# Optimization experiments

Hardware: AMD Instinct MI355X
Metric: run time of the kernel (lower is better)

The kernel has to match this reference:

```python
import jax, jax.numpy as jnp
import numpy as np

# Static config matching init_kwargs / forward constants
H = 12          # num_heads
D = 64          # head_dim
SW = 64         # kv_cache_sliding_window (frames)
SF = 8          # kv_cache_scale_frames
NUM_REG = 4     # num_register_tokens -> camera_idx=0, scale_idx=5
SPECIAL_END = NUM_REG + 2  # camera..scale inclusive slice = tokens [0:6)


def setup_inputs() -> dict:
    key = jax.random.key(0)
    ks = jax.random.split(key, 9)
    B, N, C = 1, 576, 768
    T = 192  # tokens per frame; num_frame_per_block = N // T = 3
    inp = {
        'x': jax.random.normal(ks[0], (B, N, C), jnp.float32),
        'qkv_w': jax.random.normal(ks[1], (3 * C, C), jnp.float32) * (C ** -0.5),
        'qkv_b': jax.random.normal(ks[2], (3 * C,), jnp.float32) * 0.02,
        'proj_w': jax.random.normal(ks[3], (C, C), jnp.float32) * (C ** -0.5),
        'proj_b': jax.random.normal(ks[4], (C,), jnp.float32) * 0.02,
        'k_cache': jax.random.normal(ks[5], (B, H, SW + SF, T, D), jnp.float32),
        'v_cache': jax.random.normal(ks[6], (B, H, SW + SF, T, D), jnp.float32),
        'k_special': jax.random.normal(ks[7], (B, H, 12, SPECIAL_END, D), jnp.float32),
        'v_special': jax.random.normal(ks[8], (B, H, 12, SPECIAL_END, D), jnp.float32),
    }
    return inp


def reference(x, qkv_w, qkv_b, proj_w, proj_b, k_cache, v_cache, k_special, v_special):
    B, N, C = x.shape
    T = k_cache.shape[3]           # tokens per frame
    nfb = N // T                   # num_frame_per_block (inferred, as in torch code)

    # qkv projection: (B,N,3C) -> (3,B,H,N,D)
    qkv = (x @ qkv_w.T + qkv_b).reshape(B, N, 3, H, D).transpose(2, 0, 3, 1, 4)
    q, k, v = qkv[0], qkv[1], qkv[2]   # each (B,H,N,D); q_norm/k_norm = Identity

    # Append new block frames to the cache
    k_cache = jnp.concatenate([k_cache, k.reshape(B, H, nfb, T, D)], axis=2)
    v_cache = jnp.concatenate([v_cache, v.reshape(B, H, nfb, T, D)], axis=2)

    # Sliding-window eviction (shapes chosen so this branch always fires)
    F = k_cache.shape[2]
    evict_start, evict_end = SF, F - SW   # 8 .. 11
    # cross-frame special tokens: camera..scale (tokens 0:6) of evicted frames
    new_sk = k_cache[:, :, evict_start:evict_end, :SPECIAL_END, :]
    new_sv = v_cache[:, :, evict_start:evict_end, :SPECIAL_END, :]
    k_special = jnp.concatenate([k_special, new_sk], axis=2)
    v_special = jnp.concatenate([v_special, new_sv], axis=2)
    # keep scale frames + last sliding_window frames
    k_cache = jnp.concatenate([k_cache[:, :, :SF], k_cache[:, :, -SW:]], axis=2)
    v_cache = jnp.concatenate([v_cache[:, :, :SF], v_cache[:, :, -SW:]], axis=2)

    # Flatten frames -> tokens; prepend special tokens
    k_full = jnp.concatenate([k_special.reshape(B, H, -1, D),
                              k_cache.reshape(B, H, -1, D)], axis=2)
    v_full = jnp.concatenate([v_special.reshape(B, H, -1, D),
                              v_cache.reshape(B, H, -1, D)], axis=2)

    # SDPA (no mask, no dropout, default scale 1/sqrt(D))
    scale = 1.0 / jnp.sqrt(jnp.float32(D))
    scores = jnp.einsum('bhnd,bhmd->bhnm', q, k_full) * scale
    attn = jax.nn.softmax(scores, axis=-1)
    out = jnp.einsum('bhnm,bhmd->bhnd', attn, v_full)

    out = out.transpose(0, 2, 1, 3).reshape(B, N, H * D)
    return out @ proj_w.T + proj_b
```

## Files before the change

kernel.cpp:

```cpp
#include <hip/hip_runtime.h>
#include <hip/hip_bf16.h>

#define NH    12
#define HD    64
#define NT    576
#define CC    768
#define M_TOT 13914
#define MP    13952
#define NTIL  218
#define NEW0  13338

typedef short bf16x8 __attribute__((ext_vector_type(8)));
typedef float f32x4 __attribute__((ext_vector_type(4)));
typedef float f32x16 __attribute__((ext_vector_type(16)));

#define QSCALE 0.18033688011112042f

__device__ __forceinline__ unsigned pk2(float a, float b) {
  __hip_bfloat162 h = __float22bfloat162_rn(make_float2(a, b));
  return *(unsigned*)&h;
}

__global__ __launch_bounds__(256) void cvt_all(
    const float* __restrict__ x, const float* __restrict__ wsrc,
    const float* __restrict__ pw, __hip_bfloat16* __restrict__ xb,
    __hip_bfloat16* __restrict__ wb, __hip_bfloat16* __restrict__ wph,
    __hip_bfloat16* __restrict__ wpl) {
  const int nx8 = NT * CC / 8;
  const int nw8 = 3 * CC * CC / 8;
  const int npw8 = CC * CC / 8;
  int i = blockIdx.x * 256 + threadIdx.x;
  if (i < nx8 + nw8) {
    const float* src; __hip_bfloat16* dst; int j;
    if (i < nx8) { src = x; dst = xb; j = i; }
    else { j = i - nx8; src = wsrc; dst = wb; }
    const float4 a = ((const float4*)src)[2 * j];
    const float4 b = ((const float4*)src)[2 * j + 1];
    __hip_bfloat16 t[8];
    t[0] = __float2bfloat16(a.x); t[1] = __float2bfloat16(a.y);
    t[2] = __float2bfloat16(a.z); t[3] = __float2bfloat16(a.w);
    t[4] = __float2bfloat16(b.x); t[5] = __float2bfloat16(b.y);
    t[6] = __float2bfloat16(b.z); t[7] = __float2bfloat16(b.w);
    ((uint4*)dst)[j] = *(const uint4*)t;
  } else {
    const int j = i - nx8 - nw8;
    if (j >= npw8) return;
    float v[8];
    const float4 a = ((const float4*)pw)[2 * j];
    const float4 b = ((const float4*)pw)[2 * j + 1];
    v[0] = a.x; v[1] = a.y; v[2] = a.z; v[3] = a.w;
    v[4] = b.x; v[5] = b.y; v[6] = b.z; v[7] = b.w;
    __hip_bfloat16 th[8], tl[8];
#pragma unroll
    for (int e = 0; e < 8; ++e) {
      th[e] = __float2bfloat16(v[e]);
      tl[e] = __float2bfloat16(v[e] - __bfloat162float(th[e]));
    }
    ((uint4*)wph)[j] = *(const uint4*)th;
    ((uint4*)wpl)[j] = *(const uint4*)tl;
  }
}

__device__ __forceinline__ const float* kv_src_row(
    const float* __restrict__ cache, const float* __restrict__ special,
    int h, int m) {
  if (m < 72) return special + ((size_t)h * 72 + m) * HD;
  if (m < 90) {
    const int j = m - 72;
    return cache + (((size_t)h * 72 + 8 + j / 6) * 192 + (j % 6)) * HD;
  }
  if (m < 1626) return cache + ((size_t)h * 13824 + (m - 90)) * HD;
  return cache + ((size_t)h * 13824 + 2112 + (m - 1626)) * HD;
}

#define GEMM_BLKS 324
#define VT_BLKS   2616
#define KB_BLKS   10004

__global__ __launch_bounds__(256) void qkv_and_gather(
    const __hip_bfloat16* __restrict__ xb, const __hip_bfloat16* __restrict__ wb,
    const float* __restrict__ bias, __hip_bfloat16* __restrict__ Qb,
    __hip_bfloat16* __restrict__ Kf, __hip_bfloat16* __restrict__ Vt,
    const float* __restrict__ kc, const float* __restrict__ ksp,
    const float* __restrict__ vc, const float* __restrict__ vsp) {
  __shared__ float vsf[64][68];
  const int bx = blockIdx.x;
  const int tid = threadIdx.x;

  if (bx < GEMM_BLKS) {
    const int w = tid >> 6, l = tid & 63, l15 = l & 15, lg = l >> 4;
    const int n0 = (bx % 36) * 64;
    const int mw = (bx / 36) * 64 + w * 16;

    f32x4 acc[4];
#pragma unroll
    for (int nt = 0; nt < 4; ++nt) acc[nt] = (f32x4){0.f, 0.f, 0.f, 0.f};

    const __hip_bfloat16* arow = xb + (size_t)(mw + l15) * CC + 8 * lg;
#pragma unroll 4
    for (int k0 = 0; k0 < CC; k0 += 32) {
      const bf16x8 a = *(const bf16x8*)(arow + k0);
#pragma unroll
      for (int nt = 0; nt < 4; ++nt) {
        const bf16x8 b =
            *(const bf16x8*)(wb + (size_t)(n0 + nt * 16 + l15) * CC + k0 + 8 * lg);
        acc[nt] = __builtin_amdgcn_mfma_f32_16x16x32_bf16(a, b, acc[nt], 0, 0, 0);
      }
    }
#pragma unroll
    for (int nt = 0; nt < 4; ++nt) {
      const int c = n0 + nt * 16 + l15;
      const int which = c / CC;
      const int rem = c - which * CC;
      const int hh = rem >> 6;
      const int dd = rem & 63;
      const float bc = bias[c];
#pragma unroll
      for (int r = 0; r < 4; ++r) {
        const int m = mw + 4 * lg + r;
        const float v = acc[nt][r] + bc;
        if (which == 0) {
          Qb[((size_t)hh * NT + m) * HD + dd] = __float2bfloat16(v * QSCALE);
        } else if (which == 1) {
          Kf[((size_t)hh * MP + NEW0 + m) * HD + dd] = __float2bfloat16(v);
        } else {
          Vt[((size_t)hh * HD + dd) * MP + NEW0 + m] = __float2bfloat16(v);
        }
      }
    }
  } else if (bx < GEMM_BLKS + VT_BLKS) {
    const int tv = bx - GEMM_BLKS;
    const int m0 = (tv % 218) * 64;
    const int h = tv / 218;
    if (m0 >= NEW0) return;
#pragma unroll
    for (int p = 0; p < 4; ++p) {
      const int mr = m0 + p * 16 + (tid >> 4);
      const int c4 = (tid & 15) * 4;
      float4 v = make_float4(0.f, 0.f, 0.f, 0.f);
      if (mr < NEW0) v = *(const float4*)(kv_src_row(vc, vsp, h, mr) + c4);
      *(float4*)&vsf[p * 16 + (tid >> 4)][c4] = v;
    }
    __syncthreads();
#pragma unroll
    for (int e0 = 0; e0 < 2; ++e0) {
      const int e = tid + e0 * 256;
      const int d = e >> 3;
      const int ms = (e & 7) * 8;
      __hip_bfloat16 t[8];
#pragma unroll
      for (int j = 0; j < 8; ++j) t[j] = __float2bfloat16(vsf[ms + j][d]);
      __hip_bfloat16* dst = Vt + ((size_t)h * HD + d) * MP + m0 + ms;
      if (m0 + ms + 8 <= NEW0) {
        *(uint4*)dst = *(const uint4*)t;
      } else {
#pragma unroll
        for (int j = 0; j < 8; ++j)
          if (m0 + ms + j < NEW0) dst[j] = t[j];
      }
    }
  } else {
    const int idx = (bx - GEMM_BLKS - VT_BLKS) * 256 + tid;
    const int per_h = NEW0 * 16;
    if (idx >= NH * per_h) return;
    const int h = idx / per_h;
    const int r = idx - h * per_h;
    const int m = r >> 4;
    const int dq = (r & 15) << 2;
    const float4 v = *(const float4*)(kv_src_row(kc, ksp, h, m) + dq);
    __hip_bfloat162* dst = (__hip_bfloat162*)(Kf + ((size_t)h * MP + m) * HD + dq);
    __hip_bfloat162 a, b;
    a.x = __float2bfloat16(v.x); a.y = __float2bfloat16(v.y);
    b.x = __float2bfloat16(v.z); b.y = __float2bfloat16(v.w);
    dst[0] = a; dst[1] = b;
  }
}

template <int S>
__global__ __launch_bounds__(256, 4) void attn_partial(
    const __hip_bfloat16* __restrict__ Qb, const __hip_bfloat16* __restrict__ Kf,
    const __hip_bfloat16* __restrict__ Vt, float* __restrict__ Opart,
    float2* __restrict__ mlpart) {
  __shared__ __align__(16) char lds[16384];
  char* ksb = lds;
  char* vtb = lds + 8192;

  const int tid = threadIdx.x;
  const int w = tid >> 6, l = tid & 63;
  const int l31 = l & 31, hi = l >> 5;

  const int i = blockIdx.x;
  const int per_xcd = (5 * NH * S) / 8;
  const int work = (i & 7) * per_xcd + (i >> 3);
  const int qt = work % 5;
  const int hs = work / 5;
  const int h = hs % NH;
  const int strip = hs / NH;

  const int qrow = qt * 128 + w * 32 + l31;
  const int qrc = qrow < NT ? qrow : NT - 1;

  bf16x8 qreg[4];
  {
    const __hip_bfloat16* qp = Qb + ((size_t)h * NT + qrc) * HD + 8 * hi;
#pragma unroll
    for (int s4 = 0; s4 < 4; ++s4) qreg[s4] = *(const bf16x8*)(qp + 16 * s4);
  }

  f32x16 oacc0, oacc1;
#pragma unroll
  for (int r = 0; r < 16; ++r) { oacc0[r] = 0.f; oacc1[r] = 0.f; }
  float m_run = -1e30f, l_run = 0.f;

  const __hip_bfloat16* Kh = Kf + (size_t)h * MP * HD;
  const __hip_bfloat16* Vth = Vt + (size_t)h * HD * MP;

  for (int t = strip; t < NTIL; t += S) {
    const int m0 = t * 64;
#pragma unroll
    for (int e = 0; e < 2; ++e) {
      const int c = tid + 256 * e;
      const int row = c >> 3, p = c & 7;
      const unsigned off = ((unsigned)((row << 7) | (p << 4))) ^ ((row & 7) << 4);
      const uint4 kd = *(const uint4*)(Kh + (size_t)(m0 + row) * HD + p * 8);
      const uint4 vd = *(const uint4*)(Vth + (size_t)row * MP + m0 + p * 8);
      *(uint4*)(ksb + off) = kd;
      *(uint4*)(vtb + off) = vd;
    }
    __syncthreads();

    f32x16 sc0, sc1;
#pragma unroll
    for (int r = 0; r < 16; ++r) { sc0[r] = 0.f; sc1[r] = 0.f; }
#pragma unroll
    for (int s4 = 0; s4 < 4; ++s4) {
      const int cb = 32 * s4 + 16 * hi;
      const unsigned o0 = ((unsigned)((l31 << 7) | cb)) ^ ((l31 & 7) << 4);
      const unsigned o1 = ((unsigned)(((l31 + 32) << 7) | cb)) ^ ((l31 & 7) << 4);
      const bf16x8 a0 = *(const bf16x8*)(ksb + o0);
      const bf16x8 a1 = *(const bf16x8*)(ksb + o1);
      sc0 = __builtin_amdgcn_mfma_f32_32x32x16_bf16(a0, qreg[s4], sc0, 0, 0, 0);
      sc1 = __builtin_amdgcn_mfma_f32_32x32x16_bf16(a1, qreg[s4], sc1, 0, 0, 0);
    }

    if (m0 + 64 > M_TOT) {
#pragma unroll
      for (int r = 0; r < 16; ++r) {
        const int base = (r & 3) + 8 * (r >> 2) + 4 * hi;
        if (m0 + base >= M_TOT) sc0[r] = -1e30f;
        if (m0 + 32 + base >= M_TOT) sc1[r] = -1e30f;
      }
    }

    float mt = sc0[0];
#pragma unroll
    for (int r = 1; r < 16; ++r) mt = fmaxf(mt, sc0[r]);
#pragma unroll
    for (int r = 0; r < 16; ++r) mt = fmaxf(mt, sc1[r]);
    mt = fmaxf(mt, __shfl_xor(mt, 32));

    if (__any(mt > m_run + 8.f)) {
      const float mn = fmaxf(m_run, mt);
      const float corr = exp2f(m_run - mn);
      m_run = mn;
      l_run *= corr;
#pragma unroll
      for (int r = 0; r < 16; ++r) { oacc0[r] *= corr; oacc1[r] *= corr; }
    }

    float psum = 0.f;
    unsigned W0[8], W1[8];
#pragma unroll
    for (int i2 = 0; i2 < 8; ++i2) {
      const float e0 = exp2f(sc0[2 * i2] - m_run);
      const float e1 = exp2f(sc0[2 * i2 + 1] - m_run);
      const float f0 = exp2f(sc1[2 * i2] - m_run);
      const float f1 = exp2f(sc1[2 * i2 + 1] - m_run);
      psum += (e0 + e1) + (f0 + f1);
      W0[i2] = pk2(e0, e1);
      W1[i2] = pk2(f0, f1);
    }
    psum += __shfl_xor(psum, 32);
    l_run += psum;

#pragma unroll
    for (int s4 = 0; s4 < 4; ++s4) {
      const int u = s4 & 1;
      const unsigned a0 = (s4 < 2) ? W0[4 * u + 0] : W1[4 * u + 0];
      const unsigned a1 = (s4 < 2) ? W0[4 * u + 1] : W1[4 * u + 1];
      const unsigned a2 = (s4 < 2) ? W0[4 * u + 2] : W1[4 * u + 2];
      const unsigned a3 = (s4 < 2) ? W0[4 * u + 3] : W1[4 * u + 3];
      const unsigned x0 = (unsigned)__shfl_xor((int)a0, 32);
      const unsigned x1 = (unsigned)__shfl_xor((int)a1, 32);
      const unsigned x2 = (unsigned)__shfl_xor((int)a2, 32);
      const unsigned x3 = (unsigned)__shfl_xor((int)a3, 32);
      union { unsigned u4[4]; bf16x8 v; } pa;
      pa.u4[0] = hi ? x2 : a0;
      pa.u4[1] = hi ? x3 : a1;
      pa.u4[2] = hi ? a2 : x0;
      pa.u4[3] = hi ? a3 : x1;
      const int cb = 32 * s4 + 16 * hi;
#pragma unroll
      for (int dh = 0; dh < 2; ++dh) {
        const int vr = 32 * dh + l31;
        const unsigned ov = ((unsigned)((vr << 7) | cb)) ^ ((vr & 7) << 4);
        const bf16x8 va = *(const bf16x8*)(vtb + ov);
        if (dh == 0)
          oacc0 = __builtin_amdgcn_mfma_f32_32x32x16_bf16(va, pa.v, oacc0, 0, 0, 0);
        else
          oacc1 = __builtin_amdgcn_mfma_f32_32x32x16_bf16(va, pa.v, oacc1, 0, 0, 0);
      }
    }
    __syncthreads();
  }

  if (qrow < NT) {
    float* Op = Opart + (((size_t)strip * NH + h) * NT + qrow) * HD;
#pragma unroll
    for (int g = 0; g < 4; ++g) {
      f32x4 o0 = {oacc0[4 * g], oacc0[4 * g + 1], oacc0[4 * g + 2], oacc0[4 * g + 3]};
      f32x4 o1 = {oacc1[4 * g], oacc1[4 * g + 1], oacc1[4 * g + 2], oacc1[4 * g + 3]};
      *(f32x4*)(Op + 8 * g + 4 * hi) = o0;
      *(f32x4*)(Op + 32 + 8 * g + 4 * hi) = o1;
    }
    if (hi == 0)
      mlpart[((size_t)strip * NH + h) * NT + qrow] = make_float2(m_run, l_run);
  }
}

template <int S>
__global__ __launch_bounds__(256) void attn_merge(
    const float* __restrict__ Opart, const float2* __restrict__ mlpart,
    __hip_bfloat16* __restrict__ Owh, __hip_bfloat16* __restrict__ Owl) {
  const int idx = blockIdx.x * 256 + threadIdx.x;
  if (idx >= NH * NT * HD) return;
  const int d = idx & 63;
  const int hn = idx >> 6;
  const int n = hn % NT;
  const int h = hn / NT;
  float M = -1e30f;
  float m[S], lv[S];
#pragma unroll
  for (int s = 0; s < S; ++s) {
    const float2 ml = mlpart[((size_t)s * NH + h) * NT + n];
    m[s] = ml.x; lv[s] = ml.y;
    M = fmaxf(M, m[s]);
  }
  float L = 0.f, O = 0.f;
#pragma unroll
  for (int s = 0; s < S; ++s) {
    const float e = exp2f(m[s] - M);
    L += lv[s] * e;
    O += Opart[(((size_t)s * NH + h) * NT + n) * HD + d] * e;
  }
  const float v = O / L;
  const __hip_bfloat16 hB = __float2bfloat16(v);
  const size_t o = (size_t)n * CC + h * HD + d;
  Owh[o] = hB;
  Owl[o] = __float2bfloat16(v - __bfloat162float(hB));
}

__global__ __launch_bounds__(256) void gemm_proj_mfma(
    const __hip_bfloat16* __restrict__ Ah, const __hip_bfloat16* __restrict__ Al,
    const __hip_bfloat16* __restrict__ Wh, const __hip_bfloat16* __restrict__ Wl,
    const float* __restrict__ bias, float* __restrict__ out_f) {
  const int tid = threadIdx.x;
  const int w = tid >> 6, l = tid & 63, l15 = l & 15, lg = l >> 4;
  const int n0 = blockIdx.x * 32;
  const int mw = blockIdx.y * 64 + w * 16;

  f32x4 acc[2];
#pragma unroll
  for (int nt = 0; nt < 2; ++nt) acc[nt] = (f32x4){0.f, 0.f, 0.f, 0.f};

  const __hip_bfloat16* ah = Ah + (size_t)(mw + l15) * CC + 8 * lg;
  const __hip_bfloat16* al = Al + (size_t)(mw + l15) * CC + 8 * lg;
#pragma unroll 2
  for (int k0 = 0; k0 < CC; k0 += 32) {
    const bf16x8 a0 = *(const bf16x8*)(ah + k0);
    const bf16x8 a1 = *(const bf16x8*)(al + k0);
#pragma unroll
    for (int nt = 0; nt < 2; ++nt) {
      const size_t wi = (size_t)(n0 + nt * 16 + l15) * CC + k0 + 8 * lg;
      const bf16x8 bh = *(const bf16x8*)(Wh + wi);
      const bf16x8 bl = *(const bf16x8*)(Wl + wi);
      acc[nt] = __builtin_amdgcn_mfma_f32_16x16x32_bf16(a0, bh, acc[nt], 0, 0, 0);
      acc[nt] = __builtin_amdgcn_mfma_f32_16x16x32_bf16(a0, bl, acc[nt], 0, 0, 0);
      acc[nt] = __builtin_amdgcn_mfma_f32_16x16x32_bf16(a1, bh, acc[nt], 0, 0, 0);
    }
  }
#pragma unroll
  for (int nt = 0; nt < 2; ++nt) {
    const int c = n0 + nt * 16 + l15;
    const float bc = bias[c];
#pragma unroll
    for (int r = 0; r < 4; ++r)
      out_f[(size_t)(mw + 4 * lg + r) * CC + c] = acc[nt][r] + bc;
  }
}

extern "C" void kernel_launch(void* const* d_in, const int* in_sizes, int n_in,
                              void* d_out, int out_size, void* d_ws,
                              size_t ws_size, hipStream_t stream) {
  const float* x       = (const float*)d_in[0];
  const float* qkv_w   = (const float*)d_in[1];
  const float* qkv_b   = (const float*)d_in[2];
  const float* proj_w  = (const float*)d_in[3];
  const float* proj_b  = (const float*)d_in[4];
  const float* k_cache = (const float*)d_in[5];
  const float* v_cache = (const float*)d_in[6];
  const float* k_specl = (const float*)d_in[7];
  const float* v_specl = (const float*)d_in[8];
  float* out = (float*)d_out;

  const size_t qb_bytes = (size_t)NH * NT * HD * 2;
  const size_t kv_bytes = (size_t)NH * MP * HD * 2;
  const size_t xb_bytes = (size_t)NT * CC * 2;
  const size_t wb_bytes = (size_t)3 * CC * CC * 2;
  const size_t pw_bytes = (size_t)CC * CC * 2;
  const size_t owh_bytes = (size_t)NT * CC * 2;

  auto need = [&](int S) -> size_t {
    const size_t op = (size_t)S * NH * NT * HD * 4;
    const size_t ml = (size_t)S * NH * NT * 8;
    const size_t opr = op > xb_bytes + wb_bytes ? op : xb_bytes + wb_bytes;
    return qb_bytes + 2 * kv_bytes + opr + ml + 2 * pw_bytes;
  };
  const int S = (need(16) <= ws_size) ? 16 : 8;
  const size_t op_bytes = (size_t)S * NH * NT * HD * 4;
  const size_t ml_bytes = (size_t)S * NH * NT * 8;
  const size_t opr = op_bytes > xb_bytes + wb_bytes ? op_bytes : xb_bytes + wb_bytes;

  char* ws = (char*)d_ws;
  __hip_bfloat16* Qb = (__hip_bfloat16*)ws;
  char* kf_region = ws + qb_bytes;
  __hip_bfloat16* Kf = (__hip_bfloat16*)kf_region;
  __hip_bfloat16* Vt = (__hip_bfloat16*)(kf_region + kv_bytes);
  char* opp = kf_region + 2 * kv_bytes;
  float* Opart = (float*)opp;
  __hip_bfloat16* xb = (__hip_bfloat16*)opp;
  __hip_bfloat16* wb = (__hip_bfloat16*)(opp + xb_bytes);
  float2* mlpart = (float2*)(opp + opr);
  __hip_bfloat16* wph = (__hip_bfloat16*)(opp + opr + ml_bytes);
  __hip_bfloat16* wpl = (__hip_bfloat16*)(opp + opr + ml_bytes + pw_bytes);
  __hip_bfloat16* Owh = (__hip_bfloat16*)kf_region;
  __hip_bfloat16* Owl = (__hip_bfloat16*)(kf_region + owh_bytes);

  cvt_all<<<dim3(1368), 256, 0, stream>>>(x, qkv_w, proj_w, xb, wb, wph, wpl);
  qkv_and_gather<<<dim3(GEMM_BLKS + VT_BLKS + KB_BLKS), 256, 0, stream>>>(
      xb, wb, qkv_b, Qb, Kf, Vt, k_cache, k_specl, v_cache, v_specl);
  if (S == 16) {
    attn_partial<16><<<dim3(5 * NH * 16), 256, 0, stream>>>(Qb, Kf, Vt, Opart, mlpart);
    attn_merge<16><<<dim3((NH * NT * HD + 255) / 256), 256, 0, stream>>>(
        Opart, mlpart, Owh, Owl);
  } else {
    attn_partial<8><<<dim3(5 * NH * 8), 256, 0, stream>>>(Qb, Kf, Vt, Opart, mlpart);
    attn_merge<8><<<dim3((NH * NT * HD + 255) / 256), 256, 0, stream>>>(
        Opart, mlpart, Owh, Owl);
  }
  gemm_proj_mfma<<<dim3(24, 9), 256, 0, stream>>>(Owh, Owl, wph, wpl, proj_b, out);
}
```

Measured before the change: 127.4 us.

## Use raw v_exp_f32, tree reductions, wider K gather, smaller proj GEMM tiles

Replaces exp2f with the raw v_exp_f32 instruction in attention and merge, dropping the range-handling wrapper. The serial max and sum chains in the softmax become tree reductions to shorten dependency chains. The K cache gather now handles 8 elements per thread with 16-byte bf16 stores, halving its block count. The projection GEMM moves to one 16x16 tile per wave on a 24x18 grid to get more blocks and parallelism, at the cost of less operand reuse per wave.

```diff
diff --git a/kernel.cpp b/kernel.cpp
--- a/kernel.cpp
+++ b/kernel.cpp
@@ -19,6 +19,12 @@
 __device__ __forceinline__ unsigned pk2(float a, float b) {
   __hip_bfloat162 h = __float22bfloat162_rn(make_float2(a, b));
   return *(unsigned*)&h;
+}
+
+__device__ __forceinline__ float fexp2(float x) {
+  float r;
+  asm("v_exp_f32 %0, %1" : "=v"(r) : "v"(x));
+  return r;
 }
 
 __global__ __launch_bounds__(256) void cvt_all(
@@ -75,7 +81,7 @@
 
 #define GEMM_BLKS 324
 #define VT_BLKS   2616
-#define KB_BLKS   10004
+#define KB_BLKS   5002
 
 __global__ __launch_bounds__(256) void qkv_and_gather(
     const __hip_bfloat16* __restrict__ xb, const __hip_bfloat16* __restrict__ wb,
@@ -161,18 +167,21 @@
     }
   } else {
     const int idx = (bx - GEMM_BLKS - VT_BLKS) * 256 + tid;
-    const int per_h = NEW0 * 16;
+    const int per_h = NEW0 * 8;
     if (idx >= NH * per_h) return;
     const int h = idx / per_h;
     const int r = idx - h * per_h;
-    const int m = r >> 4;
-    const int dq = (r & 15) << 2;
-    const float4 v = *(const float4*)(kv_src_row(kc, ksp, h, m) + dq);
-    __hip_bfloat162* dst = (__hip_bfloat162*)(Kf + ((size_t)h * MP + m) * HD + dq);
-    __hip_bfloat162 a, b;
-    a.x = __float2bfloat16(v.x); a.y = __float2bfloat16(v.y);
-    b.x = __float2bfloat16(v.z); b.y = __float2bfloat16(v.w);
-    dst[0] = a; dst[1] = b;
+    const int m = r >> 3;
+    const int d8 = (r & 7) << 3;
+    const float* src = kv_src_row(kc, ksp, h, m) + d8;
+    const float4 v0 = *(const float4*)src;
+    const float4 v1 = *(const float4*)(src + 4);
+    uint4 o;
+    o.x = pk2(v0.x, v0.y);
+    o.y = pk2(v0.z, v0.w);
+    o.z = pk2(v1.x, v1.y);
+    o.w = pk2(v1.z, v1.w);
+    *(uint4*)(Kf + ((size_t)h * MP + m) * HD + d8) = o;
   }
 }
 
@@ -252,34 +261,39 @@
       }
     }
 
-    float mt = sc0[0];
-#pragma unroll
-    for (int r = 1; r < 16; ++r) mt = fmaxf(mt, sc0[r]);
-#pragma unroll
-    for (int r = 0; r < 16; ++r) mt = fmaxf(mt, sc1[r]);
+    float t8[8];
+#pragma unroll
+    for (int r2 = 0; r2 < 8; ++r2)
+      t8[r2] = fmaxf(fmaxf(sc0[r2], sc0[r2 + 8]), fmaxf(sc1[r2], sc1[r2 + 8]));
+#pragma unroll
+    for (int r2 = 0; r2 < 4; ++r2) t8[r2] = fmaxf(t8[r2], t8[r2 + 4]);
+    float mt = fmaxf(fmaxf(t8[0], t8[1]), fmaxf(t8[2], t8[3]));
     mt = fmaxf(mt, __shfl_xor(mt, 32));
 
     if (__any(mt > m_run + 8.f)) {
       const float mn = fmaxf(m_run, mt);
-      const float corr = exp2f(m_run - mn);
+      const float corr = fexp2(m_run - mn);
       m_run = mn;
       l_run *= corr;
 #pragma unroll
       for (int r = 0; r < 16; ++r) { oacc0[r] *= corr; oacc1[r] *= corr; }
     }
 
-    float psum = 0.f;
     unsigned W0[8], W1[8];
+    float s8[8];
 #pragma unroll
     for (int i2 = 0; i2 < 8; ++i2) {
-      const float e0 = exp2f(sc0[2 * i2] - m_run);
-      const float e1 = exp2f(sc0[2 * i2 + 1] - m_run);
-      const float f0 = exp2f(sc1[2 * i2] - m_run);
-      const float f1 = exp2f(sc1[2 * i2 + 1] - m_run);
-      psum += (e0 + e1) + (f0 + f1);
+      const float e0 = fexp2(sc0[2 * i2] - m_run);
+      const float e1 = fexp2(sc0[2 * i2 + 1] - m_run);
+      const float f0 = fexp2(sc1[2 * i2] - m_run);
+      const float f1 = fexp2(sc1[2 * i2 + 1] - m_run);
       W0[i2] = pk2(e0, e1);
       W1[i2] = pk2(f0, f1);
-    }
+      s8[i2] = (e0 + e1) + (f0 + f1);
+    }
+#pragma unroll
+    for (int i2 = 0; i2 < 4; ++i2) s8[i2] += s8[i2 + 4];
+    float psum = (s8[0] + s8[1]) + (s8[2] + s8[3]);
     psum += __shfl_xor(psum, 32);
     l_run += psum;
 
@@ -349,7 +363,7 @@
   float L = 0.f, O = 0.f;
 #pragma unroll
   for (int s = 0; s < S; ++s) {
-    const float e = exp2f(m[s] - M);
+    const float e = fexp2(m[s] - M);
     L += lv[s] * e;
     O += Opart[(((size_t)s * NH + h) * NT + n) * HD + d] * e;
   }
@@ -366,37 +380,29 @@
     const float* __restrict__ bias, float* __restrict__ out_f) {
   const int tid = threadIdx.x;
   const int w = tid >> 6, l = tid & 63, l15 = l & 15, lg = l >> 4;
-  const int n0 = blockIdx.x * 32;
-  const int mw = blockIdx.y * 64 + w * 16;
-
-  f32x4 acc[2];
-#pragma unroll
-  for (int nt = 0; nt < 2; ++nt) acc[nt] = (f32x4){0.f, 0.f, 0.f, 0.f};
+  const int n0 = blockIdx.x * 32 + (w >> 1) * 16;
+  const int mw = blockIdx.y * 32 + (w & 1) * 16;
+
+  f32x4 acc = (f32x4){0.f, 0.f, 0.f, 0.f};
 
   const __hip_bfloat16* ah = Ah + (size_t)(mw + l15) * CC + 8 * lg;
   const __hip_bfloat16* al = Al + (size_t)(mw + l15) * CC + 8 * lg;
-#pragma unroll 2
+#pragma unroll 4
   for (int k0 = 0; k0 < CC; k0 += 32) {
     const bf16x8 a0 = *(const bf16x8*)(ah + k0);
     const bf16x8 a1 = *(const bf16x8*)(al + k0);
-#pragma unroll
-    for (int nt = 0; nt < 2; ++nt) {
-      const size_t wi = (size_t)(n0 + nt * 16 + l15) * CC + k0 + 8 * lg;
-      const bf16x8 bh = *(const bf16x8*)(Wh + wi);
-      const bf16x8 bl = *(const bf16x8*)(Wl + wi);
-      acc[nt] = __builtin_amdgcn_mfma_f32_16x16x32_bf16(a0, bh, acc[nt], 0, 0, 0);
-      acc[nt] = __builtin_amdgcn_mfma_f32_16x16x32_bf16(a0, bl, acc[nt], 0, 0, 0);
-      acc[nt] = __builtin_amdgcn_mfma_f32_16x16x32_bf16(a1, bh, acc[nt], 0, 0, 0);
-    }
-  }
-#pragma unroll
-  for (int nt = 0; nt < 2; ++nt) {
-    const int c = n0 + nt * 16 + l15;
-    const float bc = bias[c];
-#pragma unroll
-    for (int r = 0; r < 4; ++r)
-      out_f[(size_t)(mw + 4 * lg + r) * CC + c] = acc[nt][r] + bc;
-  }
+    const size_t wi = (size_t)(n0 + l15) * CC + k0 + 8 * lg;
+    const bf16x8 bh = *(const bf16x8*)(Wh + wi);
+    const bf16x8 bl = *(const bf16x8*)(Wl + wi);
+    acc = __builtin_amdgcn_mfma_f32_16x16x32_bf16(a0, bh, acc, 0, 0, 0);
+    acc = __builtin_amdgcn_mfma_f32_16x16x32_bf16(a0, bl, acc, 0, 0, 0);
+    acc = __builtin_amdgcn_mfma_f32_16x16x32_bf16(a1, bh, acc, 0, 0, 0);
+  }
+  const int c = n0 + l15;
+  const float bc = bias[c];
+#pragma unroll
+  for (int r = 0; r < 4; ++r)
+    out_f[(size_t)(mw + 4 * lg + r) * CC + c] = acc[r] + bc;
 }
 
 extern "C" void kernel_launch(void* const* d_in, const int* in_sizes, int n_in,
@@ -458,5 +464,5 @@
     attn_merge<8><<<dim3((NH * NT * HD + 255) / 256), 256, 0, stream>>>(
         Opart, mlpart, Owh, Owl);
   }
-  gemm_proj_mfma<<<dim3(24, 9), 256, 0, stream>>>(Owh, Owl, wph, wpl, proj_b, out);
-}
+  gemm_proj_mfma<<<dim3(24, 18), 256, 0, stream>>>(Owh, Owl, wph, wpl, proj_b, out);
+}
```

Result: faster. 122.7 us (-3.7%).
